# Performance work log

Hardware: AMD Instinct MI355X
Metric: run time of the kernel (lower is better)

## Reference

```python
import jax, jax.numpy as jnp
import numpy as np

HIDDEN = 100

def _lstm_step(h, c, gx, Whh, bhh):
    # gx: precomputed input contribution W_ih @ x + b_ih, shape [4H]
    gates = gx + Whh @ h + bhh
    i, f, g, o = jnp.split(gates, 4)
    i = jax.nn.sigmoid(i)
    f = jax.nn.sigmoid(f)
    g = jnp.tanh(g)
    o = jax.nn.sigmoid(o)
    c = f * c + i * g
    h = o * jnp.tanh(c)
    return h, c


def setup_inputs() -> dict:
    key = jax.random.key(0)
    ks = jax.random.split(key, 12)
    s = 0.1
    T_enc, T_dec = 4096, 4096
    return {
        "x": jax.random.normal(ks[0], (1, T_enc, 3), jnp.float32),
        "y": jax.random.randint(ks[1], (1, T_dec), 0, 6),
        "enc_Wih": jax.random.normal(ks[2], (4 * HIDDEN, 3), jnp.float32) * s,
        "enc_Whh": jax.random.normal(ks[3], (4 * HIDDEN, HIDDEN), jnp.float32) * s,
        "enc_bih": jax.random.normal(ks[4], (4 * HIDDEN,), jnp.float32) * s,
        "enc_bhh": jax.random.normal(ks[5], (4 * HIDDEN,), jnp.float32) * s,
        "dec_Wih": jax.random.normal(ks[6], (4 * HIDDEN, 1), jnp.float32) * s,
        "dec_Whh": jax.random.normal(ks[7], (4 * HIDDEN, HIDDEN), jnp.float32) * s,
        "dec_bih": jax.random.normal(ks[8], (4 * HIDDEN,), jnp.float32) * s,
        "dec_bhh": jax.random.normal(ks[9], (4 * HIDDEN,), jnp.float32) * s,
        "lin_W": jax.random.normal(ks[10], (6, HIDDEN), jnp.float32) * s,
        "lin_b": jax.random.normal(ks[11], (6,), jnp.float32) * s,
        "teacher_forcing_ratio": 1,
        "n_classes": 6,
    }


def reference(x, y, enc_Wih, enc_Whh, enc_bih, enc_bhh,
              dec_Wih, dec_Whh, dec_bih, dec_bhh, lin_W, lin_b,
              teacher_forcing_ratio, n_classes):
    T_dec = y.shape[1]
    # ---- Encoder: batch=1 LSTM over source sequence ----
    gx_enc = x[0] @ enc_Wih.T + enc_bih  # [T_enc, 4H]

    def enc_step(carry, gx):
        h, c = carry
        h, c = _lstm_step(h, c, gx, enc_Whh, enc_bhh)
        return (h, c), None

    h0 = jnp.zeros((HIDDEN,), x.dtype)
    (h_enc, c_enc), _ = jax.lax.scan(enc_step, (h0, h0), gx_enc)

    # ---- Decoder: single-step loop with teacher forcing ----
    yf = y[0].astype(jnp.float32)          # target labels fed as floats
    ratio = jnp.float32(teacher_forcing_ratio)
    u = jax.random.uniform(jax.random.key(1), (T_dec - 1,), jnp.float32)

    def dec_step(carry, inp):
        h, c, dec_in = carry
        u_t, y_t = inp
        gx = dec_in * dec_Wih[:, 0] + dec_bih  # scalar input -> [4H]
        h, c = _lstm_step(h, c, gx, dec_Whh, dec_bhh)
        logits = lin_W @ h + lin_b             # [n_classes]
        top_pred = jnp.argmax(logits).astype(jnp.float32)
        new_in = jnp.where(u_t < ratio, y_t, top_pred)
        return (h, c, new_in), logits

    _, logits_seq = jax.lax.scan(dec_step, (h_enc, c_enc, yf[0]), (u, yf[1:]))
    # outputs[0][t-1] = logits at step t, t = 1..T_dec-1; last row stays zero
    outputs = jnp.zeros((1, T_dec, n_classes), jnp.float32)
    outputs = outputs.at[0, : T_dec - 1].set(logits_seq)
    return outputs
```

## Files before the change

### kernel.cpp

```cpp
#include <hip/hip_runtime.h>

typedef _Float16 h2_t __attribute__((ext_vector_type(2)));

#define HID  100
#define TENC 4096
#define TDEC 4096
#define NCLS 6
#define NTHR 256

__device__ __forceinline__ float sigm(float v)  { return __builtin_amdgcn_rcpf(1.0f + __expf(-v)); }
__device__ __forceinline__ float tanh_(float v) { return 1.0f - 2.0f * __builtin_amdgcn_rcpf(1.0f + __expf(2.0f * v)); }

#define SYNC_LDS() asm volatile("s_waitcnt lgkmcnt(0)\n\ts_barrier" ::: "memory")

__device__ __forceinline__ float packh2(float a, float b) {
    h2_t p; p[0] = (_Float16)a; p[1] = (_Float16)b;
    return __builtin_bit_cast(float, p);
}

__device__ __forceinline__ float xsum1(float v) {
    const int s = __builtin_amdgcn_update_dpp(
        0, __builtin_bit_cast(int, v), 0xB1, 0xF, 0xF, true);
    return v + __builtin_bit_cast(float, s);
}

__global__ __launch_bounds__(NTHR, 1)
void lstm_rec(const float* __restrict__ x,
              const int*   __restrict__ y,
              const float* __restrict__ eWih,
              const float* __restrict__ eWhh,
              const float* __restrict__ ebih,
              const float* __restrict__ ebhh,
              const float* __restrict__ dWih,
              const float* __restrict__ dWhh,
              const float* __restrict__ dbih,
              const float* __restrict__ dbhh,
              float* __restrict__ hsto)
{
    __shared__ __align__(16) _Float16 hbuf[2][2][64];
    __shared__ __align__(8)  uint2    xst[TENC];
    __shared__               unsigned yst[TDEC];

    const int  t     = threadIdx.x;
    const int  w     = t >> 6;
    const int  l     = t & 63;
    const int  khalf = l & 1;
    const int  cell  = w * 32 + (l >> 1);
    const bool live  = (cell < HID);
    const int  k0    = khalf * 50;

    for (int i = t; i < TENC; i += NTHR) {
        const float a = x[3*i], b = x[3*i+1], cc = x[3*i+2];
        uint2 u;
        u.x = __builtin_bit_cast(unsigned, packh2(a, b));
        u.y = __builtin_bit_cast(unsigned, packh2(cc, 1.0f));
        xst[i] = u;
    }
    for (int i = t; i < TDEC; i += NTHR)
        yst[i] = __builtin_bit_cast(unsigned, packh2((float)y[i], 0.0f));
    if (t < 256) ((_Float16*)hbuf)[t] = (_Float16)0.0f;

    float wf[4][25];
    float wxp[4][2], bs[4];
    float c = 0.0f;
    #pragma unroll
    for (int r = 0; r < 4; ++r) {
        #pragma unroll
        for (int j = 0; j < 25; ++j) wf[r][j] = 0.0f;
        wxp[r][0] = wxp[r][1] = 0.0f; bs[r] = 0.0f;
    }
    if (live) {
        #pragma unroll
        for (int r = 0; r < 4; ++r) {
            const int row = cell + r * HID;
            #pragma unroll
            for (int j = 0; j < 25; ++j)
                wf[r][j] = packh2(eWhh[row*HID + k0 + 2*j], eWhh[row*HID + k0 + 2*j + 1]);
            if (khalf == 0) {
                wxp[r][0] = packh2(eWih[row*3+0], eWih[row*3+1]);
                wxp[r][1] = packh2(eWih[row*3+2], 0.0f);
                bs[r]     = ebih[row] + ebhh[row];
            }
        }
    }
    __syncthreads();

    const int hh2  = (cell < 50) ? 0 : 1;
    const int hoff = cell - 50 * hh2;

    int p = 0;

    for (int s = 0; s < TENC; ++s) {
        const float4* h4 = (const float4*)&hbuf[p][khalf][0];
        float hp[25];
        #pragma unroll
        for (int j = 0; j < 6; ++j) {
            const float4 v = h4[j];
            hp[4*j+0] = v.x; hp[4*j+1] = v.y; hp[4*j+2] = v.z; hp[4*j+3] = v.w;
        }
        hp[24] = ((const float*)h4)[24];

        const uint2 xp = xst[s];
        const h2_t x0 = __builtin_bit_cast(h2_t, xp.x);
        const h2_t x1 = __builtin_bit_cast(h2_t, xp.y);
        float a0 = __builtin_amdgcn_fdot2(__builtin_bit_cast(h2_t, wxp[0][0]), x0,
                   __builtin_amdgcn_fdot2(__builtin_bit_cast(h2_t, wxp[0][1]), x1, bs[0], false), false);
        float a1 = __builtin_amdgcn_fdot2(__builtin_bit_cast(h2_t, wxp[1][0]), x0,
                   __builtin_amdgcn_fdot2(__builtin_bit_cast(h2_t, wxp[1][1]), x1, bs[1], false), false);
        float a2 = __builtin_amdgcn_fdot2(__builtin_bit_cast(h2_t, wxp[2][0]), x0,
                   __builtin_amdgcn_fdot2(__builtin_bit_cast(h2_t, wxp[2][1]), x1, bs[2], false), false);
        float a3 = __builtin_amdgcn_fdot2(__builtin_bit_cast(h2_t, wxp[3][0]), x0,
                   __builtin_amdgcn_fdot2(__builtin_bit_cast(h2_t, wxp[3][1]), x1, bs[3], false), false);

        #pragma unroll
        for (int j = 0; j < 25; ++j) {
            const h2_t hh = __builtin_bit_cast(h2_t, hp[j]);
            a0 = __builtin_amdgcn_fdot2(__builtin_bit_cast(h2_t, wf[0][j]), hh, a0, false);
            a1 = __builtin_amdgcn_fdot2(__builtin_bit_cast(h2_t, wf[1][j]), hh, a1, false);
            a2 = __builtin_amdgcn_fdot2(__builtin_bit_cast(h2_t, wf[2][j]), hh, a2, false);
            a3 = __builtin_amdgcn_fdot2(__builtin_bit_cast(h2_t, wf[3][j]), hh, a3, false);
        }

        a0 = xsum1(a0);
        a1 = xsum1(a1);
        a2 = xsum1(a2);
        a3 = xsum1(a3);

        const float fi = sigm(a0), ff = sigm(a1), fg = tanh_(a2), fo = sigm(a3);
        c = ff * c + fi * fg;
        const float hn = fo * tanh_(c);
        if (khalf == 0 && live)
            hbuf[p ^ 1][hh2][hoff] = (_Float16)hn;
        SYNC_LDS();
        p ^= 1;
    }

    float wdp[4], bsd[4];
    #pragma unroll
    for (int r = 0; r < 4; ++r) { wdp[r] = 0.0f; bsd[r] = 0.0f; }
    if (live) {
        #pragma unroll
        for (int r = 0; r < 4; ++r) {
            const int row = cell + r * HID;
            #pragma unroll
            for (int j = 0; j < 25; ++j)
                wf[r][j] = packh2(dWhh[row*HID + k0 + 2*j], dWhh[row*HID + k0 + 2*j + 1]);
            if (khalf == 0) {
                wdp[r] = packh2(dWih[row], 0.0f);
                bsd[r] = dbih[row] + dbhh[row];
            }
        }
    }

    for (int s = 0; s < TDEC - 1; ++s) {
        const float4* h4 = (const float4*)&hbuf[p][khalf][0];
        float hp[25];
        #pragma unroll
        for (int j = 0; j < 6; ++j) {
            const float4 v = h4[j];
            hp[4*j+0] = v.x; hp[4*j+1] = v.y; hp[4*j+2] = v.z; hp[4*j+3] = v.w;
        }
        hp[24] = ((const float*)h4)[24];

        const h2_t yp = __builtin_bit_cast(h2_t, yst[s]);
        float a0 = __builtin_amdgcn_fdot2(__builtin_bit_cast(h2_t, wdp[0]), yp, bsd[0], false);
        float a1 = __builtin_amdgcn_fdot2(__builtin_bit_cast(h2_t, wdp[1]), yp, bsd[1], false);
        float a2 = __builtin_amdgcn_fdot2(__builtin_bit_cast(h2_t, wdp[2]), yp, bsd[2], false);
        float a3 = __builtin_amdgcn_fdot2(__builtin_bit_cast(h2_t, wdp[3]), yp, bsd[3], false);

        #pragma unroll
        for (int j = 0; j < 25; ++j) {
            const h2_t hh = __builtin_bit_cast(h2_t, hp[j]);
            a0 = __builtin_amdgcn_fdot2(__builtin_bit_cast(h2_t, wf[0][j]), hh, a0, false);
            a1 = __builtin_amdgcn_fdot2(__builtin_bit_cast(h2_t, wf[1][j]), hh, a1, false);
            a2 = __builtin_amdgcn_fdot2(__builtin_bit_cast(h2_t, wf[2][j]), hh, a2, false);
            a3 = __builtin_amdgcn_fdot2(__builtin_bit_cast(h2_t, wf[3][j]), hh, a3, false);
        }

        a0 = xsum1(a0);
        a1 = xsum1(a1);
        a2 = xsum1(a2);
        a3 = xsum1(a3);

        const float fi = sigm(a0), ff = sigm(a1), fg = tanh_(a2), fo = sigm(a3);
        c = ff * c + fi * fg;
        const float hn = fo * tanh_(c);
        if (live) {
            if (khalf == 0) {
                hbuf[p ^ 1][hh2][hoff] = (_Float16)hn;
            } else {
                hsto[s * HID + cell] = hn;
            }
        }
        SYNC_LDS();
        p ^= 1;
    }
}

__global__ __launch_bounds__(256)
void logits_k(const float* __restrict__ hsto, const float* __restrict__ linW,
              const float* __restrict__ linb, float* __restrict__ out)
{
    const int idx = blockIdx.x * 256 + threadIdx.x;
    if (idx >= TDEC * NCLS) return;
    const int tt = idx / NCLS;
    const int r  = idx % NCLS;
    if (tt >= TDEC - 1) { out[idx] = 0.0f; return; }
    const float* h  = hsto + tt * HID;
    const float* wr = linW + r * HID;
    float a = linb[r];
    #pragma unroll 4
    for (int k = 0; k < HID; ++k) a += wr[k] * h[k];
    out[idx] = a;
}

extern "C" void kernel_launch(void* const* d_in, const int* in_sizes, int n_in,
                              void* d_out, int out_size, void* d_ws, size_t ws_size,
                              hipStream_t stream)
{
    const float* x    = (const float*)d_in[0];
    const int*   y    = (const int*)  d_in[1];
    const float* eWih = (const float*)d_in[2];
    const float* eWhh = (const float*)d_in[3];
    const float* ebih = (const float*)d_in[4];
    const float* ebhh = (const float*)d_in[5];
    const float* dWih = (const float*)d_in[6];
    const float* dWhh = (const float*)d_in[7];
    const float* dbih = (const float*)d_in[8];
    const float* dbhh = (const float*)d_in[9];
    const float* linW = (const float*)d_in[10];
    const float* linb = (const float*)d_in[11];
    float* out  = (float*)d_out;
    float* hsto = (float*)d_ws;

    lstm_rec<<<dim3(1), dim3(NTHR), 0, stream>>>(
        x, y, eWih, eWhh, ebih, ebhh, dWih, dWhh, dbih, dbhh, hsto);

    const int nout = TDEC * NCLS;
    logits_k<<<dim3((nout + 255) / 256), dim3(256), 0, stream>>>(hsto, linW, linb, out);
}
```

Before: 3.495 ms.

## Compute LSTM recurrent matvec with MFMA tiles and fold input/bias into K

Replaces the per-thread fdot2 matvec, with its DPP cross-lane reduction, by 16x16x32 f16 MFMA instructions. Weights are laid out as gate-interleaved A tiles in registers, and the h vector is broadcast as the B operand from LDS. The input features and the bias are appended to the K dimension as extra h-buffer entries, so the separate input projection is dropped. The aim is to shorten the per-step serial latency of the recurrence. The cost is mostly wasted MFMA columns, a tile-selection step, and extra register pressure from 28 f16x8 weight tiles.

```diff
diff --git a/kernel.cpp b/kernel.cpp
--- a/kernel.cpp
+++ b/kernel.cpp
@@ -1,6 +1,8 @@
 #include <hip/hip_runtime.h>
 
-typedef _Float16 h2_t __attribute__((ext_vector_type(2)));
+typedef _Float16 h2_t  __attribute__((ext_vector_type(2)));
+typedef _Float16 f16x8 __attribute__((ext_vector_type(8)));
+typedef float    f32x4 __attribute__((ext_vector_type(4)));
 
 #define HID  100
 #define TENC 4096
@@ -16,12 +18,6 @@
 __device__ __forceinline__ float packh2(float a, float b) {
     h2_t p; p[0] = (_Float16)a; p[1] = (_Float16)b;
     return __builtin_bit_cast(float, p);
-}
-
-__device__ __forceinline__ float xsum1(float v) {
-    const int s = __builtin_amdgcn_update_dpp(
-        0, __builtin_bit_cast(int, v), 0xB1, 0xF, 0xF, true);
-    return v + __builtin_bit_cast(float, s);
 }
 
 __global__ __launch_bounds__(NTHR, 1)
@@ -37,17 +33,18 @@
               const float* __restrict__ dbhh,
               float* __restrict__ hsto)
 {
-    __shared__ __align__(16) _Float16 hbuf[2][2][64];
+    __shared__ __align__(16) _Float16 hbuf[2][128];
     __shared__ __align__(8)  uint2    xst[TENC];
     __shared__               unsigned yst[TDEC];
 
-    const int  t     = threadIdx.x;
-    const int  w     = t >> 6;
-    const int  l     = t & 63;
-    const int  khalf = l & 1;
-    const int  cell  = w * 32 + (l >> 1);
-    const bool live  = (cell < HID);
-    const int  k0    = khalf * 50;
+    const int t   = threadIdx.x;
+    const int w   = t >> 6;
+    const int l   = t & 63;
+    const int col = l & 15;
+    const int lg  = l >> 4;
+    const int nt   = (w == 0) ? 7 : 6;
+    const int base = (w == 0) ? 0 : 7 + (w - 1) * 6;
+    const int gate = col & 3;
 
     for (int i = t; i < TENC; i += NTHR) {
         const float a = x[3*i], b = x[3*i+1], cc = x[3*i+2];
@@ -59,138 +56,152 @@
     for (int i = t; i < TDEC; i += NTHR)
         yst[i] = __builtin_bit_cast(unsigned, packh2((float)y[i], 0.0f));
     if (t < 256) ((_Float16*)hbuf)[t] = (_Float16)0.0f;
-
-    float wf[4][25];
-    float wxp[4][2], bs[4];
+    __syncthreads();
+
+    if (t == 0) {
+        uint2 u;
+        u.x = __builtin_bit_cast(unsigned, packh2(x[0], x[1]));
+        u.y = __builtin_bit_cast(unsigned, packh2(x[2], 1.0f));
+        *(uint2*)&hbuf[0][100] = u;
+    }
+
+    f16x8 wA[7][4];
+    #pragma unroll
+    for (int tt = 0; tt < 7; ++tt) {
+        #pragma unroll
+        for (int kt = 0; kt < 4; ++kt) {
+            f16x8 a;
+            #pragma unroll
+            for (int j = 0; j < 8; ++j) {
+                float v = 0.0f;
+                if (tt < nt) {
+                    const int cellA = 4*(base + tt) + (col >> 2);
+                    const int wrow  = gate * HID + cellA;
+                    const int k     = 32*kt + 8*lg + j;
+                    if (k < HID)            v = eWhh[wrow*HID + k];
+                    else if (k < HID + 3)   v = eWih[wrow*3 + (k - HID)];
+                    else if (k == HID + 3)  v = ebih[wrow] + ebhh[wrow];
+                }
+                a[j] = (_Float16)v;
+            }
+            wA[tt][kt] = a;
+        }
+    }
+    SYNC_LDS();
+
+    int ts = col;
+    if (ts >= nt) ts -= nt;
+    if (ts >= nt) ts -= nt;
+    const int cell = 4*(base + ts) + lg;
+
     float c = 0.0f;
-    #pragma unroll
-    for (int r = 0; r < 4; ++r) {
-        #pragma unroll
-        for (int j = 0; j < 25; ++j) wf[r][j] = 0.0f;
-        wxp[r][0] = wxp[r][1] = 0.0f; bs[r] = 0.0f;
-    }
-    if (live) {
-        #pragma unroll
-        for (int r = 0; r < 4; ++r) {
-            const int row = cell + r * HID;
-            #pragma unroll
-            for (int j = 0; j < 25; ++j)
-                wf[r][j] = packh2(eWhh[row*HID + k0 + 2*j], eWhh[row*HID + k0 + 2*j + 1]);
-            if (khalf == 0) {
-                wxp[r][0] = packh2(eWih[row*3+0], eWih[row*3+1]);
-                wxp[r][1] = packh2(eWih[row*3+2], 0.0f);
-                bs[r]     = ebih[row] + ebhh[row];
-            }
-        }
-    }
-    __syncthreads();
-
-    const int hh2  = (cell < 50) ? 0 : 1;
-    const int hoff = cell - 50 * hh2;
-
     int p = 0;
 
     for (int s = 0; s < TENC; ++s) {
-        const float4* h4 = (const float4*)&hbuf[p][khalf][0];
-        float hp[25];
-        #pragma unroll
-        for (int j = 0; j < 6; ++j) {
-            const float4 v = h4[j];
-            hp[4*j+0] = v.x; hp[4*j+1] = v.y; hp[4*j+2] = v.z; hp[4*j+3] = v.w;
-        }
-        hp[24] = ((const float*)h4)[24];
-
-        const uint2 xp = xst[s];
-        const h2_t x0 = __builtin_bit_cast(h2_t, xp.x);
-        const h2_t x1 = __builtin_bit_cast(h2_t, xp.y);
-        float a0 = __builtin_amdgcn_fdot2(__builtin_bit_cast(h2_t, wxp[0][0]), x0,
-                   __builtin_amdgcn_fdot2(__builtin_bit_cast(h2_t, wxp[0][1]), x1, bs[0], false), false);
-        float a1 = __builtin_amdgcn_fdot2(__builtin_bit_cast(h2_t, wxp[1][0]), x0,
-                   __builtin_amdgcn_fdot2(__builtin_bit_cast(h2_t, wxp[1][1]), x1, bs[1], false), false);
-        float a2 = __builtin_amdgcn_fdot2(__builtin_bit_cast(h2_t, wxp[2][0]), x0,
-                   __builtin_amdgcn_fdot2(__builtin_bit_cast(h2_t, wxp[2][1]), x1, bs[2], false), false);
-        float a3 = __builtin_amdgcn_fdot2(__builtin_bit_cast(h2_t, wxp[3][0]), x0,
-                   __builtin_amdgcn_fdot2(__builtin_bit_cast(h2_t, wxp[3][1]), x1, bs[3], false), false);
-
-        #pragma unroll
-        for (int j = 0; j < 25; ++j) {
-            const h2_t hh = __builtin_bit_cast(h2_t, hp[j]);
-            a0 = __builtin_amdgcn_fdot2(__builtin_bit_cast(h2_t, wf[0][j]), hh, a0, false);
-            a1 = __builtin_amdgcn_fdot2(__builtin_bit_cast(h2_t, wf[1][j]), hh, a1, false);
-            a2 = __builtin_amdgcn_fdot2(__builtin_bit_cast(h2_t, wf[2][j]), hh, a2, false);
-            a3 = __builtin_amdgcn_fdot2(__builtin_bit_cast(h2_t, wf[3][j]), hh, a3, false);
-        }
-
-        a0 = xsum1(a0);
-        a1 = xsum1(a1);
-        a2 = xsum1(a2);
-        a3 = xsum1(a3);
-
-        const float fi = sigm(a0), ff = sigm(a1), fg = tanh_(a2), fo = sigm(a3);
+        const f16x8* hb = (const f16x8*)hbuf[p];
+        const f16x8 B0 = hb[ 0 + lg];
+        const f16x8 B1 = hb[ 4 + lg];
+        const f16x8 B2 = hb[ 8 + lg];
+        const f16x8 B3 = hb[12 + lg];
+
+        if (t == 0 && s + 1 < TENC)
+            *(uint2*)&hbuf[p ^ 1][100] = xst[s + 1];
+
+        f32x4 acc[7];
+        #pragma unroll
+        for (int tt = 0; tt < 7; ++tt) {
+            if (tt < nt) {
+                f32x4 z = {0.0f, 0.0f, 0.0f, 0.0f};
+                z = __builtin_amdgcn_mfma_f32_16x16x32_f16(wA[tt][0], B0, z, 0, 0, 0);
+                z = __builtin_amdgcn_mfma_f32_16x16x32_f16(wA[tt][1], B1, z, 0, 0, 0);
+                z = __builtin_amdgcn_mfma_f32_16x16x32_f16(wA[tt][2], B2, z, 0, 0, 0);
+                z = __builtin_amdgcn_mfma_f32_16x16x32_f16(wA[tt][3], B3, z, 0, 0, 0);
+                acc[tt] = z;
+            }
+        }
+
+        f32x4 q = acc[0];
+        #pragma unroll
+        for (int tt = 1; tt < 7; ++tt)
+            if (tt < nt && ts == tt) q = acc[tt];
+
+        const float fi = sigm(q[0]), ff = sigm(q[1]), fg = tanh_(q[2]), fo = sigm(q[3]);
         c = ff * c + fi * fg;
         const float hn = fo * tanh_(c);
-        if (khalf == 0 && live)
-            hbuf[p ^ 1][hh2][hoff] = (_Float16)hn;
+        if (col < nt)
+            hbuf[p ^ 1][cell] = (_Float16)hn;
         SYNC_LDS();
         p ^= 1;
     }
 
-    float wdp[4], bsd[4];
+    if (t == 0) {
+        uint2 v;
+        v.x = (yst[0] & 0xFFFFu) | 0x3C000000u;
+        v.y = 0u;
+        *(uint2*)&hbuf[p][100] = v;
+    }
+
     #pragma unroll
-    for (int r = 0; r < 4; ++r) { wdp[r] = 0.0f; bsd[r] = 0.0f; }
-    if (live) {
-        #pragma unroll
-        for (int r = 0; r < 4; ++r) {
-            const int row = cell + r * HID;
+    for (int tt = 0; tt < 7; ++tt) {
+        #pragma unroll
+        for (int kt = 0; kt < 4; ++kt) {
+            f16x8 a;
             #pragma unroll
-            for (int j = 0; j < 25; ++j)
-                wf[r][j] = packh2(dWhh[row*HID + k0 + 2*j], dWhh[row*HID + k0 + 2*j + 1]);
-            if (khalf == 0) {
-                wdp[r] = packh2(dWih[row], 0.0f);
-                bsd[r] = dbih[row] + dbhh[row];
-            }
-        }
-    }
+            for (int j = 0; j < 8; ++j) {
+                float v = 0.0f;
+                if (tt < nt) {
+                    const int cellA = 4*(base + tt) + (col >> 2);
+                    const int wrow  = gate * HID + cellA;
+                    const int k     = 32*kt + 8*lg + j;
+                    if (k < HID)            v = dWhh[wrow*HID + k];
+                    else if (k == HID)      v = dWih[wrow];
+                    else if (k == HID + 1)  v = dbih[wrow] + dbhh[wrow];
+                }
+                a[j] = (_Float16)v;
+            }
+            wA[tt][kt] = a;
+        }
+    }
+    SYNC_LDS();
 
     for (int s = 0; s < TDEC - 1; ++s) {
-        const float4* h4 = (const float4*)&hbuf[p][khalf][0];
-        float hp[25];
-        #pragma unroll
-        for (int j = 0; j < 6; ++j) {
-            const float4 v = h4[j];
-            hp[4*j+0] = v.x; hp[4*j+1] = v.y; hp[4*j+2] = v.z; hp[4*j+3] = v.w;
-        }
-        hp[24] = ((const float*)h4)[24];
-
-        const h2_t yp = __builtin_bit_cast(h2_t, yst[s]);
-        float a0 = __builtin_amdgcn_fdot2(__builtin_bit_cast(h2_t, wdp[0]), yp, bsd[0], false);
-        float a1 = __builtin_amdgcn_fdot2(__builtin_bit_cast(h2_t, wdp[1]), yp, bsd[1], false);
-        float a2 = __builtin_amdgcn_fdot2(__builtin_bit_cast(h2_t, wdp[2]), yp, bsd[2], false);
-        float a3 = __builtin_amdgcn_fdot2(__builtin_bit_cast(h2_t, wdp[3]), yp, bsd[3], false);
-
-        #pragma unroll
-        for (int j = 0; j < 25; ++j) {
-            const h2_t hh = __builtin_bit_cast(h2_t, hp[j]);
-            a0 = __builtin_amdgcn_fdot2(__builtin_bit_cast(h2_t, wf[0][j]), hh, a0, false);
-            a1 = __builtin_amdgcn_fdot2(__builtin_bit_cast(h2_t, wf[1][j]), hh, a1, false);
-            a2 = __builtin_amdgcn_fdot2(__builtin_bit_cast(h2_t, wf[2][j]), hh, a2, false);
-            a3 = __builtin_amdgcn_fdot2(__builtin_bit_cast(h2_t, wf[3][j]), hh, a3, false);
-        }
-
-        a0 = xsum1(a0);
-        a1 = xsum1(a1);
-        a2 = xsum1(a2);
-        a3 = xsum1(a3);
-
-        const float fi = sigm(a0), ff = sigm(a1), fg = tanh_(a2), fo = sigm(a3);
+        const f16x8* hb = (const f16x8*)hbuf[p];
+        const f16x8 B0 = hb[ 0 + lg];
+        const f16x8 B1 = hb[ 4 + lg];
+        const f16x8 B2 = hb[ 8 + lg];
+        const f16x8 B3 = hb[12 + lg];
+
+        if (t == 0 && s + 1 < TDEC - 1) {
+            uint2 v;
+            v.x = (yst[s + 1] & 0xFFFFu) | 0x3C000000u;
+            v.y = 0u;
+            *(uint2*)&hbuf[p ^ 1][100] = v;
+        }
+
+        f32x4 acc[7];
+        #pragma unroll
+        for (int tt = 0; tt < 7; ++tt) {
+            if (tt < nt) {
+                f32x4 z = {0.0f, 0.0f, 0.0f, 0.0f};
+                z = __builtin_amdgcn_mfma_f32_16x16x32_f16(wA[tt][0], B0, z, 0, 0, 0);
+                z = __builtin_amdgcn_mfma_f32_16x16x32_f16(wA[tt][1], B1, z, 0, 0, 0);
+                z = __builtin_amdgcn_mfma_f32_16x16x32_f16(wA[tt][2], B2, z, 0, 0, 0);
+                z = __builtin_amdgcn_mfma_f32_16x16x32_f16(wA[tt][3], B3, z, 0, 0, 0);
+                acc[tt] = z;
+            }
+        }
+
+        f32x4 q = acc[0];
+        #pragma unroll
+        for (int tt = 1; tt < 7; ++tt)
+            if (tt < nt && ts == tt) q = acc[tt];
+
+        const float fi = sigm(q[0]), ff = sigm(q[1]), fg = tanh_(q[2]), fo = sigm(q[3]);
         c = ff * c + fi * fg;
         const float hn = fo * tanh_(c);
-        if (live) {
-            if (khalf == 0) {
-                hbuf[p ^ 1][hh2][hoff] = (_Float16)hn;
-            } else {
-                hsto[s * HID + cell] = hn;
-            }
+        if (col < nt) {
+            hbuf[p ^ 1][cell] = (_Float16)hn;
+            hsto[s * HID + cell] = hn;
         }
         SYNC_LDS();
         p ^= 1;
```

After: 4.179 ms. 1.2x slower.
